# Performance work log

Hardware: AMD Instinct MI355X
Metric: run time of the kernel (lower is better)

## Reference

```python
import jax, jax.numpy as jnp
import numpy as np

# One irrep per degree l = 0..7 -> irreps.dim = sum(2l+1) = 64
IRREPS = [0, 1, 2, 3, 4, 5, 6, 7]


def _build_indices(ls):
    # Enumerate (irrep_idx, l, m) in order, matching z_rotation_infos.
    m_list = []
    for ii, l in enumerate(ls):
        for m in range(-l, l + 1):
            m_list.append((ii, l, m))
    lm = {t: i for i, t in enumerate(m_list)}
    dim = len(m_list)
    c_idx = np.zeros(dim, np.int32)   # index into cs for the cos factor (0 -> constant 1)
    s_idx = np.zeros(dim, np.int32)   # index into cs for the sin factor
    sign = np.zeros(dim, np.float32)  # -sign(m) coefficient carrier (0 for m==0)
    neg = np.zeros(dim, np.int32)     # flat index of the (l, -m) partner component
    for M, (ii, l, m) in enumerate(m_list):
        if m == 0:
            c_idx[M] = 0          # cs[:,0] == 1.0
            s_idx[M] = 0
            sign[M] = 0.0
            neg[M] = M
        else:
            am = abs(m)
            c_idx[M] = 2 * am      # cos(|m| phi)
            s_idx[M] = 2 * am - 1  # sin(|m| phi)
            sign[M] = 1.0 if m > 0 else -1.0
            neg[M] = lm[(ii, l, -m)]
    return dim, c_idx, s_idx, sign, neg


DIM, C_IDX, S_IDX, SIGN, NEG = _build_indices(IRREPS)
MAX_M = max(IRREPS)


def prepare_sincos(angle, max_m):
    # cs layout: [1, sin(phi), cos(phi), sin(2phi), cos(2phi), ...] -> (N, 1 + 2*max_m)
    m = jnp.arange(1, max_m + 1, dtype=angle.dtype)
    ma = angle[:, None] * m                                   # (N, max_m)
    sc = jnp.stack([jnp.sin(ma), jnp.cos(ma)], axis=-1)       # (N, max_m, 2)
    sc = sc.reshape(angle.shape[0], 2 * max_m)
    ones = jnp.ones((angle.shape[0], 1), dtype=angle.dtype)
    return jnp.concatenate([ones, sc], axis=-1)


def setup_inputs() -> dict:
    key = jax.random.key(0)
    k1, k2 = jax.random.split(key)
    N, C = 50000, 64
    inp = jax.random.normal(k1, (N, DIM, C), dtype=jnp.float32)
    angle = jax.random.normal(k2, (N,), dtype=jnp.float32)
    return {"input": inp, "angle": angle}


def reference(input, angle):
    # out[n,M,c] = cos(|m|phi_n) * x[n,M,c] - sign(m) * sin(|m|phi_n) * x[n, (l,-m), c]
    # (m == 0 rows: cos factor is cs[:,0]==1 and sign==0, i.e. identity)
    cs = prepare_sincos(angle, MAX_M)          # (N, 1 + 2*MAX_M)
    cos_t = cs[:, C_IDX][:, :, None]           # (N, DIM, 1)
    sin_t = cs[:, S_IDX][:, :, None]           # (N, DIM, 1)
    sign = jnp.asarray(SIGN)[None, :, None]
    return cos_t * input - sign * sin_t * input[:, NEG, :]
```

## Files before the change

kernel.cpp:

```cpp
#include <hip/hip_runtime.h>

__constant__ int c_am[64] = {
  0,
  1,0,1,
  2,1,0,1,2,
  3,2,1,0,1,2,3,
  4,3,2,1,0,1,2,3,4,
  5,4,3,2,1,0,1,2,3,4,5,
  6,5,4,3,2,1,0,1,2,3,4,5,6,
  7,6,5,4,3,2,1,0,1,2,3,4,5,6,7
};
__constant__ float c_sign[64] = {
  0.f,
  -1.f,0.f,1.f,
  -1.f,-1.f,0.f,1.f,1.f,
  -1.f,-1.f,-1.f,0.f,1.f,1.f,1.f,
  -1.f,-1.f,-1.f,-1.f,0.f,1.f,1.f,1.f,1.f,
  -1.f,-1.f,-1.f,-1.f,-1.f,0.f,1.f,1.f,1.f,1.f,1.f,
  -1.f,-1.f,-1.f,-1.f,-1.f,-1.f,0.f,1.f,1.f,1.f,1.f,1.f,1.f,
  -1.f,-1.f,-1.f,-1.f,-1.f,-1.f,-1.f,0.f,1.f,1.f,1.f,1.f,1.f,1.f,1.f
};
__constant__ int c_neg[64] = {
  0,
  3,2,1,
  8,7,6,5,4,
  15,14,13,12,11,10,9,
  24,23,22,21,20,19,18,17,16,
  35,34,33,32,31,30,29,28,27,26,25,
  48,47,46,45,44,43,42,41,40,39,38,37,36,
  63,62,61,60,59,58,57,56,55,54,53,52,51,50,49
};

__global__ __launch_bounds__(256) void wigner_z_kernel(
    const float4* __restrict__ x, const float* __restrict__ angle,
    float4* __restrict__ out, int N) {
  __shared__ float s_sin[8];
  __shared__ float s_cos[8];

  const int n = blockIdx.x;
  if (n >= N) return;
  const int t = threadIdx.x;

  if (t < 8) {
    float s, c;
    sincosf((float)t * angle[n], &s, &c);
    s_sin[t] = s;
    s_cos[t] = c;
  }
  __syncthreads();

  const float4* xb = x + (size_t)n * 1024;
  float4* ob = out + (size_t)n * 1024;

#pragma unroll
  for (int k = 0; k < 4; ++k) {
    const int f = t + k * 256;
    const int M = f >> 4;
    const int c4 = f & 15;
    const int am = c_am[M];
    const float co = s_cos[am];
    const float si = c_sign[M] * s_sin[am];

    const float4 a = xb[f];
    const float4 b = xb[(c_neg[M] << 4) | c4];

    float4 o;
    o.x = co * a.x - si * b.x;
    o.y = co * a.y - si * b.y;
    o.z = co * a.z - si * b.z;
    o.w = co * a.w - si * b.w;
    ob[f] = o;
  }
}

extern "C" void kernel_launch(void* const* d_in, const int* in_sizes, int n_in,
                              void* d_out, int out_size, void* d_ws, size_t ws_size,
                              hipStream_t stream) {
  const float4* x = (const float4*)d_in[0];
  const float* angle = (const float*)d_in[1];
  float4* out = (float4*)d_out;
  const int N = in_sizes[1];

  wigner_z_kernel<<<N, 256, 0, stream>>>(x, angle, out, N);
}
```

Baseline: 291.1 us.

## Process (m,-m) component pairs per thread to load each input once

Restructures the work so each thread loads the +m and -m components together and writes both rotated outputs. The m=0 rows are handled by a separate set of threads as a plain copy. This removes the duplicate read of each partner row and the sign lookups, cutting cache and load traffic. Blocks grow to 576 threads, which changes occupancy granularity.

```diff
diff --git a/kernel.cpp b/kernel.cpp
--- a/kernel.cpp
+++ b/kernel.cpp
@@ -1,44 +1,25 @@
 #include <hip/hip_runtime.h>
 
-__constant__ int c_am[64] = {
-  0,
-  1,0,1,
-  2,1,0,1,2,
-  3,2,1,0,1,2,3,
-  4,3,2,1,0,1,2,3,4,
-  5,4,3,2,1,0,1,2,3,4,5,
-  6,5,4,3,2,1,0,1,2,3,4,5,6,
-  7,6,5,4,3,2,1,0,1,2,3,4,5,6,7
+__constant__ int P_A[28] = {
+  3, 7,8, 13,14,15, 21,22,23,24, 31,32,33,34,35,
+  43,44,45,46,47,48, 57,58,59,60,61,62,63
 };
-__constant__ float c_sign[64] = {
-  0.f,
-  -1.f,0.f,1.f,
-  -1.f,-1.f,0.f,1.f,1.f,
-  -1.f,-1.f,-1.f,0.f,1.f,1.f,1.f,
-  -1.f,-1.f,-1.f,-1.f,0.f,1.f,1.f,1.f,1.f,
-  -1.f,-1.f,-1.f,-1.f,-1.f,0.f,1.f,1.f,1.f,1.f,1.f,
-  -1.f,-1.f,-1.f,-1.f,-1.f,-1.f,0.f,1.f,1.f,1.f,1.f,1.f,1.f,
-  -1.f,-1.f,-1.f,-1.f,-1.f,-1.f,-1.f,0.f,1.f,1.f,1.f,1.f,1.f,1.f,1.f
+__constant__ int P_B[28] = {
+  1, 5,4, 11,10,9, 19,18,17,16, 29,28,27,26,25,
+  41,40,39,38,37,36, 55,54,53,52,51,50,49
 };
-__constant__ int c_neg[64] = {
-  0,
-  3,2,1,
-  8,7,6,5,4,
-  15,14,13,12,11,10,9,
-  24,23,22,21,20,19,18,17,16,
-  35,34,33,32,31,30,29,28,27,26,25,
-  48,47,46,45,44,43,42,41,40,39,38,37,36,
-  63,62,61,60,59,58,57,56,55,54,53,52,51,50,49
+__constant__ int P_AM[28] = {
+  1, 1,2, 1,2,3, 1,2,3,4, 1,2,3,4,5, 1,2,3,4,5,6, 1,2,3,4,5,6,7
 };
+__constant__ int S_R[8] = {0,2,6,12,20,30,42,56};
 
-__global__ __launch_bounds__(256) void wigner_z_kernel(
+__global__ __launch_bounds__(576) void wigner_z_pair_kernel(
     const float4* __restrict__ x, const float* __restrict__ angle,
     float4* __restrict__ out, int N) {
   __shared__ float s_sin[8];
   __shared__ float s_cos[8];
 
   const int n = blockIdx.x;
-  if (n >= N) return;
   const int t = threadIdx.x;
 
   if (t < 8) {
@@ -49,27 +30,36 @@
   }
   __syncthreads();
 
-  const float4* xb = x + (size_t)n * 1024;
-  float4* ob = out + (size_t)n * 1024;
+  const float4* __restrict__ xb = x + (size_t)n * 1024;
+  float4* __restrict__ ob = out + (size_t)n * 1024;
 
-#pragma unroll
-  for (int k = 0; k < 4; ++k) {
-    const int f = t + k * 256;
-    const int M = f >> 4;
-    const int c4 = f & 15;
-    const int am = c_am[M];
+  if (t < 448) {
+    const int p = t >> 4;
+    const int c4 = t & 15;
+    const int fa = (P_A[p] << 4) | c4;
+    const int fb = (P_B[p] << 4) | c4;
+    const int am = P_AM[p];
     const float co = s_cos[am];
-    const float si = c_sign[M] * s_sin[am];
+    const float si = s_sin[am];
 
-    const float4 a = xb[f];
-    const float4 b = xb[(c_neg[M] << 4) | c4];
+    const float4 a = xb[fa];
+    const float4 b = xb[fb];
 
-    float4 o;
-    o.x = co * a.x - si * b.x;
-    o.y = co * a.y - si * b.y;
-    o.z = co * a.z - si * b.z;
-    o.w = co * a.w - si * b.w;
-    ob[f] = o;
+    float4 oa, obv;
+    oa.x = co * a.x - si * b.x;
+    oa.y = co * a.y - si * b.y;
+    oa.z = co * a.z - si * b.z;
+    oa.w = co * a.w - si * b.w;
+    obv.x = co * b.x + si * a.x;
+    obv.y = co * b.y + si * a.y;
+    obv.z = co * b.z + si * a.z;
+    obv.w = co * b.w + si * a.w;
+    ob[fa] = oa;
+    ob[fb] = obv;
+  } else {
+    const int q = t - 448;
+    const int f = (S_R[q >> 4] << 4) | (q & 15);
+    ob[f] = xb[f];
   }
 }
 
@@ -81,5 +71,5 @@
   float4* out = (float4*)d_out;
   const int N = in_sizes[1];
 
-  wigner_z_kernel<<<N, 256, 0, stream>>>(x, angle, out, N);
+  wigner_z_pair_kernel<<<N, 576, 0, stream>>>(x, angle, out, N);
 }
```

New measurement: 276.1 us. 5.2% less time.
